# Optimization experiments

Hardware: AMD Instinct MI355X
Metric: run time of the kernel (lower is better)

## Reference

```python
import jax, jax.numpy as jnp
import numpy as np

R = 2          # pool ratio -> context window = R * P
P = 8          # patch_size
STRIDE = 8     # window_stride
NH = 8         # n_heads
EPS = 1e-6


def _partition_nonoverlap(x, ws):
    # (N,C,H,W) -> (N*nH*nW, C, ws, ws), matches F.unfold path with padding 0
    n, c, h, w = x.shape
    x = x.reshape(n, c, h // ws, ws, w // ws, ws)
    x = jnp.transpose(x, (0, 2, 4, 1, 3, 5))
    return x.reshape(-1, c, ws, ws)


def _partition_overlap(x, ws, stride):
    # (N,C,H,W) -> (N*nH*nW, C, ws, ws) with padding (ws-stride)//2, matching F.unfold
    n, c, h, w = x.shape
    pad = (ws - stride) // 2
    xp = jnp.pad(x, ((0, 0), (0, 0), (pad, pad), (pad, pad)))
    ih = (jnp.arange(h // stride) * stride)[:, None] + jnp.arange(ws)[None, :]
    iw = (jnp.arange(w // stride) * stride)[:, None] + jnp.arange(ws)[None, :]
    xw = xp[:, :, ih, :]          # (n, c, nH, ws, Wp)
    xw = xw[:, :, :, :, iw]       # (n, c, nH, ws, nW, ws)
    xw = jnp.transpose(xw, (0, 2, 4, 1, 3, 5))  # (n, nH, nW, c, ws, ws)
    return xw.reshape(-1, c, ws, ws)


def setup_inputs() -> dict:
    key = jax.random.key(0)
    ks = jax.random.split(key, 4)
    C = 512
    x = jax.random.normal(ks[0], (1, C, 128, 128), jnp.float32)
    ln_w = jnp.ones((C,), jnp.float32)
    ln_b = jnp.zeros((C,), jnp.float32)
    mix_w = jax.random.normal(ks[1], (NH, P * P, P * P), jnp.float32) * 0.02
    mix_b = jnp.zeros((NH, P * P), jnp.float32)
    in_w = jax.random.normal(ks[2], (3 * C, C), jnp.float32) * 0.02
    in_b = jnp.zeros((3 * C,), jnp.float32)
    out_w = jax.random.normal(ks[3], (C, C), jnp.float32) * 0.02
    out_b = jnp.zeros((C,), jnp.float32)
    return dict(x=x, ln_w=ln_w, ln_b=ln_b, mix_w=mix_w, mix_b=mix_b,
                in_w=in_w, in_b=in_b, out_w=out_w, out_b=out_b)


def reference(x, ln_w, ln_b, mix_w, mix_b, in_w, in_b, out_w, out_b):
    n, c, h, w = x.shape
    ws = R * P
    L = P * P  # 64 positions per window

    # query windows: non-overlapping 8x8 patches -> (B, L, C)
    q = _partition_nonoverlap(x, P)
    q = q.reshape(-1, c, L).transpose(0, 2, 1)

    # context windows: 16x16 overlapping, avg-pooled r x r -> 8x8 -> (B, L, C)
    ctx = _partition_overlap(x, ws, STRIDE)
    ctx = ctx.reshape(-1, c, P, R, P, R).mean(axis=(3, 5))  # AvgPool2d(r, r)
    ctx = ctx.reshape(-1, c, L).transpose(0, 2, 1)

    # LayerNorm over channel dim (eps 1e-6, biased variance)
    mu = ctx.mean(-1, keepdims=True)
    var = ctx.var(-1, keepdims=True)
    ctx = (ctx - mu) / jnp.sqrt(var + EPS) * ln_w + ln_b

    # PositionMixing: per-head Linear(64,64) over the L axis + residual
    B = ctx.shape[0]
    t = ctx.transpose(0, 2, 1).reshape(B, NH, c // NH, L)  # (B, H, hd, L)
    mixed = jnp.einsum('bhcl,hml->bhcm', t, mix_w) + mix_b[None, :, None, :]
    ctx = (t + mixed).reshape(B, c, L).transpose(0, 2, 1)  # (B, L, C)

    # nn.MultiheadAttention with batch_first=False (torch default):
    # first dim B (windows) is the SEQUENCE, second dim L=64 is the BATCH.
    hd = c // NH
    Wq, Wk, Wv = in_w[:c], in_w[c:2 * c], in_w[2 * c:]
    bq, bk, bv = in_b[:c], in_b[c:2 * c], in_b[2 * c:]
    Q = (jnp.einsum('slc,ec->sle', q, Wq) + bq).reshape(B, L, NH, hd)
    K = (jnp.einsum('slc,ec->sle', ctx, Wk) + bk).reshape(B, L, NH, hd)
    V = (jnp.einsum('slc,ec->sle', ctx, Wv) + bv).reshape(B, L, NH, hd)
    scale = 1.0 / jnp.sqrt(jnp.asarray(hd, x.dtype))
    scores = jnp.einsum('slhd,tlhd->lhst', Q, K) * scale  # (L, H, B, B)
    attn = jax.nn.softmax(scores, axis=-1)
    o = jnp.einsum('lhst,tlhd->slhd', attn, V).reshape(B, L, c)
    o = jnp.einsum('slc,ec->sle', o, out_w) + out_b

    # nlc_to_nchw + window_reverse -> (N, C, H, W)
    o = o.transpose(0, 2, 1).reshape(B, c, P, P)
    o = o.reshape(n, h // P, w // P, c, P, P)
    o = jnp.transpose(o, (0, 3, 1, 4, 2, 5)).reshape(n, c, h, w)
    return o
```

## Files before the change

### kernel.cpp

```cpp
#include <hip/hip_runtime.h>


typedef __bf16 bf16;
typedef __bf16 bf16x2 __attribute__((ext_vector_type(2)));
typedef __bf16 bf16x4 __attribute__((ext_vector_type(4)));
typedef __bf16 bf16x8 __attribute__((ext_vector_type(8)));
typedef float f32x4 __attribute__((ext_vector_type(4)));

#define MFMA(a, b, c) __builtin_amdgcn_mfma_f32_16x16x32_bf16(a, b, c, 0, 0, 0)

__device__ __forceinline__ void gll16(const void* g, void* l) {
  __builtin_amdgcn_global_load_lds((const __attribute__((address_space(1))) void*)g,
                                   (__attribute__((address_space(3))) void*)l, 16, 0, 0);
}

__global__ void k_wconv(const float* __restrict__ in_w, const float* __restrict__ out_w,
                        bf16* __restrict__ wib, bf16* __restrict__ wob) {
  int i = blockIdx.x * blockDim.x + threadIdx.x;
  const int n1 = (1536 * 512) / 4;
  float4 v;
  bf16* dst;
  if (i < n1) { v = ((const float4*)in_w)[i];      dst = wib + (size_t)i * 4; }
  else        { v = ((const float4*)out_w)[i - n1]; dst = wob + (size_t)(i - n1) * 4; }
  dst[0] = (bf16)v.x; dst[1] = (bf16)v.y; dst[2] = (bf16)v.z; dst[3] = (bf16)v.w;
}

__global__ __launch_bounds__(256) void k_pq(const float* __restrict__ x,
                                            float* __restrict__ xp2t,
                                            bf16* __restrict__ qb) {
  __shared__ float xs[2][64][133];
  const int y2 = blockIdx.x, c0 = blockIdx.y * 64, t = threadIdx.x;
  #pragma unroll
  for (int it = 0; it < 16; ++it) {
    int flat = it * 256 + t;
    int ci = flat >> 6, rest = flat & 63;
    int yb = rest >> 5, xq = rest & 31;
    float4 v = *(const float4*)(x + (size_t)(c0 + ci) * 16384 +
                                (size_t)(2 * y2 + yb) * 128 + xq * 4);
    float* d = &xs[yb][ci][xq * 4];
    d[0] = v.x; d[1] = v.y; d[2] = v.z; d[3] = v.w;
  }
  __syncthreads();
  #pragma unroll
  for (int it = 0; it < 16; ++it) {
    int flat = it * 256 + t;
    int x2 = flat >> 6, ci = flat & 63;
    float s = xs[0][ci][2 * x2] + xs[0][ci][2 * x2 + 1] +
              xs[1][ci][2 * x2] + xs[1][ci][2 * x2 + 1];
    xp2t[(size_t)(y2 * 64 + x2) * 512 + c0 + ci] = 0.25f * s;
  }
  #pragma unroll
  for (int yb = 0; yb < 2; ++yb) {
    const int Y = 2 * y2 + yb;
    const int hy = Y >> 3, py = Y & 7;
    #pragma unroll
    for (int it = 0; it < 32; ++it) {
      int flat = it * 256 + t;
      int X = flat >> 6, ci = flat & 63;
      int l = py * 8 + (X & 7), s = hy * 16 + (X >> 3);
      qb[((size_t)l * 256 + s) * 512 + c0 + ci] = (bf16)xs[yb][ci][X];
    }
  }
}

__global__ __launch_bounds__(512) void k_ln(const float* __restrict__ xp2t,
                                            const float* __restrict__ lnw,
                                            const float* __restrict__ lnb,
                                            bf16* __restrict__ T) {
  __shared__ bf16 Tt[512][24];
  const int s = blockIdx.x, qt = blockIdx.y;
  const int wy = s >> 4, wx = s & 15;
  const int t = threadIdx.x, wv = t >> 6, ln = t & 63;

  float wl[8], bl[8];
  #pragma unroll
  for (int k = 0; k < 8; ++k) { wl[k] = lnw[k * 64 + ln]; bl[k] = lnb[k * 64 + ln]; }

  float v[2][8], mu_[2], rs_[2];
  #pragma unroll
  for (int p = 0; p < 2; ++p) {
    const int l = qt * 16 + wv * 2 + p;
    const int py = l >> 3, px = l & 7;
    const int y2 = wy * 4 - 2 + py, x2 = wx * 4 - 2 + px;
    const bool inb = (y2 >= 0) && (y2 < 64) && (x2 >= 0) && (x2 < 64);
    const float* src = xp2t + (size_t)(y2 * 64 + x2) * 512;
    float sum = 0.f, ssq = 0.f;
    #pragma unroll
    for (int k = 0; k < 8; ++k) {
      float xv = 0.f;
      if (inb) xv = src[k * 64 + ln];
      v[p][k] = xv; sum += xv; ssq += xv * xv;
    }
    #pragma unroll
    for (int off = 1; off < 64; off <<= 1) {
      sum += __shfl_xor(sum, off);
      ssq += __shfl_xor(ssq, off);
    }
    float mu = sum * (1.f / 512.f);
    mu_[p] = mu;
    rs_[p] = rsqrtf(ssq * (1.f / 512.f) - mu * mu + 1e-6f);
  }
  #pragma unroll
  for (int k = 0; k < 8; ++k) {
    const int c = k * 64 + ln;
    bf16x2 u;
    u.x = (bf16)((v[0][k] - mu_[0]) * rs_[0] * wl[k] + bl[k]);
    u.y = (bf16)((v[1][k] - mu_[1]) * rs_[1] * wl[k] + bl[k]);
    *(bf16x2*)(&Tt[c][wv * 2]) = u;
  }
  __syncthreads();
  #pragma unroll
  for (int it = 0; it < 2; ++it) {
    int flat = it * 512 + t;
    int c = flat >> 1, ch = flat & 1;
    bf16x8 u = *(const bf16x8*)(&Tt[c][ch * 8]);
    *(bf16x8*)(T + ((size_t)s * 512 + c) * 64 + qt * 16 + ch * 8) = u;
  }
}

__global__ __launch_bounds__(256) void k_mix(const bf16* __restrict__ T,
                                             const float* __restrict__ mix_w,
                                             const float* __restrict__ mix_b,
                                             bf16* __restrict__ ctx) {
  const int t = threadIdx.x, wv = t >> 6, ln = t & 63;
  const int s = blockIdx.x, hg = blockIdx.y;
  const int h = hg * 4 + wv;
  const int q = ln >> 4, r = ln & 15;

  bf16x8 a[4][2];
  #pragma unroll
  for (int m = 0; m < 4; ++m) {
    #pragma unroll
    for (int ks = 0; ks < 2; ++ks) {
      const int rm = m * 16 + r;
      const float* wsrc = mix_w + ((size_t)h * 64 + rm) * 64 + ks * 32 + q * 8;
      bf16x8 pk;
      #pragma unroll
      for (int e = 0; e < 8; ++e) {
        int l = ks * 32 + q * 8 + e;
        float w = wsrc[e] + (rm == l ? 1.f : 0.f);
        pk[e] = (bf16)w;
      }
      a[m][ks] = pk;
    }
  }
  const bf16* Tb = T + ((size_t)s * 512 + h * 64) * 64;
  bf16x8 b[4][2];
  #pragma unroll
  for (int n = 0; n < 4; ++n) {
    #pragma unroll
    for (int ks = 0; ks < 2; ++ks)
      b[n][ks] = *(const bf16x8*)(Tb + (size_t)(n * 16 + r) * 64 + ks * 32 + q * 8);
  }
  f32x4 acc[4][4] = {};
  #pragma unroll
  for (int ks = 0; ks < 2; ++ks) {
    #pragma unroll
    for (int m = 0; m < 4; ++m) {
      #pragma unroll
      for (int n = 0; n < 4; ++n) acc[m][n] = MFMA(a[m][ks], b[n][ks], acc[m][n]);
    }
  }
  #pragma unroll
  for (int m = 0; m < 4; ++m) {
    #pragma unroll
    for (int j = 0; j < 4; ++j) {
      const int rm = m * 16 + q * 4 + j;
      const float bias = mix_b[h * 64 + rm];
      #pragma unroll
      for (int n = 0; n < 4; ++n)
        ctx[((size_t)rm * 256 + s) * 512 + h * 64 + n * 16 + r] =
            (bf16)(acc[m][n][j] + bias);
    }
  }
}

template <int MODE>
__global__ __launch_bounds__(256, 4) void k_gemm(const bf16* __restrict__ A,
                                                 const bf16* __restrict__ B,
                                                 const float* __restrict__ bias,
                                                 bf16* __restrict__ O0,
                                                 bf16* __restrict__ O1) {
  __shared__ bf16 As[8192];
  __shared__ bf16 Bs[8192];
  const int t = threadIdx.x, wv = t >> 6, ln = t & 63;
  const int bm = blockIdx.x, bn = blockIdx.y;
  const int wm = wv >> 1, wn = wv & 1;
  const int q = ln >> 4, r = ln & 15;
  f32x4 acc[4][4] = {};

  const int srow = wv * 8 + (ln >> 3);
  const int swzc = (ln & 7) ^ (ln >> 3);
  const char* ga = (const char*)A + ((size_t)(bm * 128 + srow) * 512) * 2 + swzc * 16;
  const char* gb = (const char*)B + ((size_t)(bn * 128 + srow) * 512) * 2 + swzc * 16;

  for (int k0 = 0; k0 < 512; k0 += 64) {
    #pragma unroll
    for (int i = 0; i < 4; ++i) {
      gll16(ga + (size_t)i * 32 * 1024 + k0 * 2, As + i * 2048 + wv * 512);
      gll16(gb + (size_t)i * 32 * 1024 + k0 * 2, Bs + i * 2048 + wv * 512);
    }
    __syncthreads();
    #pragma unroll
    for (int ks = 0; ks < 2; ++ks) {
      bf16x8 af[4], bfr[4];
      #pragma unroll
      for (int m = 0; m < 4; ++m)
        af[m] = *(const bf16x8*)(As + (wm * 64 + m * 16 + r) * 64 +
                                 (((ks * 4 + q) ^ (r & 7)) * 8));
      #pragma unroll
      for (int n = 0; n < 4; ++n)
        bfr[n] = *(const bf16x8*)(Bs + (wn * 64 + n * 16 + r) * 64 +
                                  (((ks * 4 + q) ^ (r & 7)) * 8));
      #pragma unroll
      for (int m = 0; m < 4; ++m) {
        #pragma unroll
        for (int n = 0; n < 4; ++n) acc[m][n] = MFMA(af[m], bfr[n], acc[m][n]);
      }
    }
    __syncthreads();
  }

  const int r0 = bm * 128 + wm * 64 + q * 4;
  const int c0 = bn * 128 + wn * 64 + r;
  #pragma unroll
  for (int m = 0; m < 4; ++m) {
    const int rg0 = r0 + m * 16;
    #pragma unroll
    for (int n = 0; n < 4; ++n) {
      const int cg = c0 + n * 16;
      const float bv = bias[cg];
      if constexpr (MODE == 2) {
        #pragma unroll
        for (int j = 0; j < 4; ++j)
          O0[(size_t)(rg0 + j) * 512 + cg] = (bf16)(acc[m][n][j] + bv);
      } else if constexpr (MODE == 0) {
        const int li = rg0 >> 8;
        #pragma unroll
        for (int j = 0; j < 4; ++j) {
          int sp = (rg0 + j) & 255;
          O0[(((size_t)li * 8 + (cg >> 6)) * 256 + sp) * 64 + (cg & 63)] =
              (bf16)(acc[m][n][j] + bv);
        }
      } else {
        const int li = rg0 >> 8;
        if (cg < 512) {
          #pragma unroll
          for (int j = 0; j < 4; ++j) {
            int sp = (rg0 + j) & 255;
            O0[(((size_t)li * 8 + (cg >> 6)) * 256 + sp) * 64 + (cg & 63)] =
                (bf16)(acc[m][n][j] + bv);
          }
        } else {
          const int e = cg - 512, hh = e >> 6, d = e & 63;
          const int sp = rg0 & 255;
          bf16x4 pk;
          #pragma unroll
          for (int j = 0; j < 4; ++j) pk[j] = (bf16)(acc[m][n][j] + bv);
          *(bf16x4*)(&O1[(((size_t)li * 8 + hh) * 64 + d) * 256 + sp]) = pk;
        }
      }
    }
  }
}

__global__ __launch_bounds__(256, 4) void k_attn(const bf16* __restrict__ Qa,
                                                 const bf16* __restrict__ Ka,
                                                 const bf16* __restrict__ Vt,
                                                 bf16* __restrict__ Oa) {
  __shared__ bf16 Ks[128][68];
  __shared__ bf16 Ps[64][132];
  __shared__ float sfl[64];
  __shared__ float rrs[64];

  const int t = threadIdx.x, wv = t >> 6, ln = t & 63;
  const int q = ln >> 4, r = ln & 15;
  const int bid = blockIdx.x;
  const int st = (bid >> 3) & 3;
  const int lh = (bid & 7) | ((bid >> 5) << 3);
  const int s0 = st * 64;
  const size_t base = (size_t)lh * (256 * 64);
  const bf16* Qlh = Qa + base;
  const bf16* Klh = Ka + base;
  const bf16* Vlh = Vt + base;

  const float SC = 0.125f * 1.4426950408889634f;

  bf16x8 aq[2];
  #pragma unroll
  for (int ks = 0; ks < 2; ++ks)
    aq[ks] = *(const bf16x8*)(Qlh + (size_t)(s0 + wv * 16 + r) * 64 + ks * 32 + q * 8);

  const int krow = t >> 1, khf = (t & 1) * 32;
  {
    bf16x8 kst0[4];
    #pragma unroll
    for (int i = 0; i < 4; ++i)
      kst0[i] = *(const bf16x8*)(Klh + (size_t)krow * 64 + khf + i * 8);
    #pragma unroll
    for (int i = 0; i < 4; ++i) *(bf16x8*)(&Ks[krow][khf + i * 8]) = kst0[i];
  }
  __syncthreads();

  f32x4 ao[4] = {};
  float m4[4], l4[4];
  f32x4 acc[8];

  #pragma unroll
  for (int n = 0; n < 8; ++n) acc[n] = (f32x4){0.f, 0.f, 0.f, 0.f};
  __builtin_amdgcn_s_setprio(1);
  #pragma unroll
  for (int n = 0; n < 8; ++n) {
    bf16x8 b0 = *(const bf16x8*)(&Ks[n * 16 + r][q * 8]);
    bf16x8 b1 = *(const bf16x8*)(&Ks[n * 16 + r][32 + q * 8]);
    acc[n] = MFMA(aq[0], b0, acc[n]);
    acc[n] = MFMA(aq[1], b1, acc[n]);
  }
  __builtin_amdgcn_s_setprio(0);

  bf16x8 bv[4];
  #pragma unroll
  for (int ks = 0; ks < 4; ++ks)
    bv[ks] = *(const bf16x8*)(Vlh + (size_t)(wv * 16 + r) * 256 + ks * 32 + q * 8);
  bf16x8 kst[4];
  #pragma unroll
  for (int i = 0; i < 4; ++i)
    kst[i] = *(const bf16x8*)(Klh + (size_t)(128 + krow) * 64 + khf + i * 8);

  #pragma unroll
  for (int j = 0; j < 4; ++j) {
    float mx = acc[0][j];
    #pragma unroll
    for (int n = 1; n < 8; ++n) mx = fmaxf(mx, acc[n][j]);
    #pragma unroll
    for (int off = 1; off < 16; off <<= 1) mx = fmaxf(mx, __shfl_xor(mx, off));
    m4[j] = mx;
    const float ms = mx * SC;
    float sm = 0.f;
    #pragma unroll
    for (int n = 0; n < 8; ++n) {
      float p = exp2f(acc[n][j] * SC - ms);
      acc[n][j] = p;
      sm += p;
    }
    #pragma unroll
    for (int off = 1; off < 16; off <<= 1) sm += __shfl_xor(sm, off);
    l4[j] = sm;
    const int row = wv * 16 + q * 4 + j;
    #pragma unroll
    for (int n = 0; n < 8; ++n) Ps[row][n * 16 + r] = (bf16)acc[n][j];
  }
  __syncthreads();

  #pragma unroll
  for (int i = 0; i < 4; ++i) *(bf16x8*)(&Ks[krow][khf + i * 8]) = kst[i];
  __builtin_amdgcn_s_setprio(1);
  #pragma unroll
  for (int ks = 0; ks < 4; ++ks) {
    #pragma unroll
    for (int m = 0; m < 4; ++m) {
      bf16x8 ap = *(const bf16x8*)(&Ps[m * 16 + r][ks * 32 + q * 8]);
      ao[m] = MFMA(ap, bv[ks], ao[m]);
    }
  }
  __builtin_amdgcn_s_setprio(0);
  __syncthreads();

  #pragma unroll
  for (int n = 0; n < 8; ++n) acc[n] = (f32x4){0.f, 0.f, 0.f, 0.f};
  __builtin_amdgcn_s_setprio(1);
  #pragma unroll
  for (int n = 0; n < 8; ++n) {
    bf16x8 b0 = *(const bf16x8*)(&Ks[n * 16 + r][q * 8]);
    bf16x8 b1 = *(const bf16x8*)(&Ks[n * 16 + r][32 + q * 8]);
    acc[n] = MFMA(aq[0], b0, acc[n]);
    acc[n] = MFMA(aq[1], b1, acc[n]);
  }
  __builtin_amdgcn_s_setprio(0);
  #pragma unroll
  for (int ks = 0; ks < 4; ++ks)
    bv[ks] = *(const bf16x8*)(Vlh + (size_t)(wv * 16 + r) * 256 + 128 + ks * 32 + q * 8);

  float sf4[4], rr4[4];
  #pragma unroll
  for (int j = 0; j < 4; ++j) {
    float mx = acc[0][j];
    #pragma unroll
    for (int n = 1; n < 8; ++n) mx = fmaxf(mx, acc[n][j]);
    #pragma unroll
    for (int off = 1; off < 16; off <<= 1) mx = fmaxf(mx, __shfl_xor(mx, off));
    const float mn = fmaxf(m4[j], mx);
    const float sf = exp2f((m4[j] - mn) * SC);
    const float ms = mn * SC;
    float sm = 0.f;
    #pragma unroll
    for (int n = 0; n < 8; ++n) {
      float p = exp2f(acc[n][j] * SC - ms);
      acc[n][j] = p;
      sm += p;
    }
    #pragma unroll
    for (int off = 1; off < 16; off <<= 1) sm += __shfl_xor(sm, off);
    sf4[j] = sf;
    rr4[j] = 1.f / (l4[j] * sf + sm);
    const int row = wv * 16 + q * 4 + j;
    #pragma unroll
    for (int n = 0; n < 8; ++n) Ps[row][n * 16 + r] = (bf16)acc[n][j];
  }
  if (r == 0) {
    *(f32x4*)(&sfl[wv * 16 + q * 4]) = (f32x4){sf4[0], sf4[1], sf4[2], sf4[3]};
    *(f32x4*)(&rrs[wv * 16 + q * 4]) = (f32x4){rr4[0], rr4[1], rr4[2], rr4[3]};
  }
  __syncthreads();

  #pragma unroll
  for (int m = 0; m < 4; ++m) {
    f32x4 sv = *(const f32x4*)(&sfl[m * 16 + q * 4]);
    #pragma unroll
    for (int j = 0; j < 4; ++j) ao[m][j] *= sv[j];
  }
  __builtin_amdgcn_s_setprio(1);
  #pragma unroll
  for (int ks = 0; ks < 4; ++ks) {
    #pragma unroll
    for (int m = 0; m < 4; ++m) {
      bf16x8 ap = *(const bf16x8*)(&Ps[m * 16 + r][ks * 32 + q * 8]);
      ao[m] = MFMA(ap, bv[ks], ao[m]);
    }
  }
  __builtin_amdgcn_s_setprio(0);

  float(*FS)[68] = (float(*)[68])(&Ks[0][0]);
  #pragma unroll
  for (int m = 0; m < 4; ++m) {
    f32x4 rv = *(const f32x4*)(&rrs[m * 16 + q * 4]);
    #pragma unroll
    for (int j = 0; j < 4; ++j)
      FS[m * 16 + q * 4 + j][wv * 16 + r] = ao[m][j] * rv[j];
  }
  __syncthreads();

  {
    const int row = t >> 2, qq = t & 3;
    const float* srcp = &FS[row][qq * 16];
    bf16x8 o0, o1;
    #pragma unroll
    for (int i = 0; i < 8; ++i) o0[i] = (bf16)srcp[i];
    #pragma unroll
    for (int i = 0; i < 8; ++i) o1[i] = (bf16)srcp[8 + i];
    bf16* dst = Oa + ((size_t)(lh >> 3) * 256 + s0 + row) * 512 + (lh & 7) * 64 + qq * 16;
    *(bf16x8*)(dst) = o0;
    *(bf16x8*)(dst + 8) = o1;
  }
}

__global__ void k_orelay(const bf16* __restrict__ o_tmp, float* __restrict__ out) {
  __shared__ bf16 buf[64][130];
  const int hy = blockIdx.x, py = blockIdx.y, e0 = blockIdx.z * 64, t = threadIdx.x;
  #pragma unroll
  for (int i = 0; i < 32; ++i) {
    int flat = i * 256 + t;
    int r = flat >> 6, e = flat & 63;
    int px = r >> 4, hx = r & 15;
    buf[e][hx * 8 + px] =
        o_tmp[((size_t)(py * 8 + px) * 256 + hy * 16 + hx) * 512 + e0 + e];
  }
  __syncthreads();
  const int Y = hy * 8 + py;
  #pragma unroll
  for (int i = 0; i < 32; ++i) {
    int flat = i * 256 + t;
    int e = flat >> 7, X = flat & 127;
    out[(size_t)(e0 + e) * 16384 + (size_t)Y * 128 + X] = (float)buf[e][X];
  }
}

extern "C" void kernel_launch(void* const* d_in, const int* in_sizes, int n_in,
                              void* d_out, int out_size, void* d_ws, size_t ws_size,
                              hipStream_t stream) {
  const float* x     = (const float*)d_in[0];
  const float* ln_w  = (const float*)d_in[1];
  const float* ln_b  = (const float*)d_in[2];
  const float* mix_w = (const float*)d_in[3];
  const float* mix_b = (const float*)d_in[4];
  const float* in_w  = (const float*)d_in[5];
  const float* in_b  = (const float*)d_in[6];
  const float* out_w = (const float*)d_in[7];
  const float* out_b = (const float*)d_in[8];
  float* out = (float*)d_out;
  char* ws = (char*)d_ws;

  const size_t MB = 1u << 20;
  float* xp2t = (float*)(ws);
  bf16* qb    = (bf16*)(ws + 8 * MB);
  bf16* Tn    = (bf16*)(ws + 24 * MB);
  bf16* ctxb  = (bf16*)(ws + 40 * MB);
  bf16* Qa    = (bf16*)(ws + 56 * MB);
  bf16* Ka    = (bf16*)(ws);
  bf16* Vt    = (bf16*)(ws + 16 * MB);
  bf16* oatt  = (bf16*)(ws + 32 * MB);
  bf16* otmp  = (bf16*)(ws + 48 * MB);
  bf16* wib   = (bf16*)(ws + 72 * MB);
  bf16* wob   = (bf16*)(ws + 72 * MB + 1572864);

  k_wconv<<<1024, 256, 0, stream>>>(in_w, out_w, wib, wob);
  k_pq<<<dim3(64, 8), 256, 0, stream>>>(x, xp2t, qb);
  k_ln<<<dim3(256, 4), 512, 0, stream>>>(xp2t, ln_w, ln_b, Tn);
  k_mix<<<dim3(256, 2), 256, 0, stream>>>(Tn, mix_w, mix_b, ctxb);
  k_gemm<0><<<dim3(128, 4), 256, 0, stream>>>(qb, wib, in_b, Qa, nullptr);
  k_gemm<1><<<dim3(128, 8), 256, 0, stream>>>(ctxb, wib + 512 * 512, in_b + 512, Ka, Vt);
  k_attn<<<2048, 256, 0, stream>>>(Qa, Ka, Vt, oatt);
  k_gemm<2><<<dim3(128, 4), 256, 0, stream>>>(oatt, wob, out_b, otmp, nullptr);
  k_orelay<<<dim3(16, 8, 8), 256, 0, stream>>>(otmp, out);
}
```

Measured before the change: 138.1 us.

## Merge Q and KV projection GEMMs into one launch; restructure attention into 4-chunk double-buffered loop

The Q projection and the K/V projection GEMMs are merged into a single launch with a 12-wide grid, where blocks choose their inputs by blockIdx.y. This removes one launch and lets the two GEMMs share the GPU. The attention kernel now processes keys in four 64-key chunks with a double-buffered K tile in shared memory and an online softmax. This shrinks LDS and register use so occupancy can rise to 5 blocks per CU, at the cost of more barriers and more rescaling steps per block.

```diff
diff --git a/kernel.cpp b/kernel.cpp
--- a/kernel.cpp
+++ b/kernel.cpp
@@ -175,12 +175,98 @@
   }
 }
 
-template <int MODE>
-__global__ __launch_bounds__(256, 4) void k_gemm(const bf16* __restrict__ A,
-                                                 const bf16* __restrict__ B,
-                                                 const float* __restrict__ bias,
-                                                 bf16* __restrict__ O0,
-                                                 bf16* __restrict__ O1) {
+__global__ __launch_bounds__(256, 4) void k_gemmQKV(const bf16* __restrict__ qb,
+                                                    const bf16* __restrict__ ctxb,
+                                                    const bf16* __restrict__ wib,
+                                                    const float* __restrict__ in_b,
+                                                    bf16* __restrict__ Qa,
+                                                    bf16* __restrict__ Ka,
+                                                    bf16* __restrict__ Vt) {
+  __shared__ bf16 As[8192];
+  __shared__ bf16 Bs[8192];
+  const int t = threadIdx.x, wv = t >> 6, ln = t & 63;
+  const int bm = blockIdx.x, bny = blockIdx.y;
+  const bool isQ = (bny < 4);
+  const int bn = isQ ? bny : bny - 4;
+  const bf16* A = isQ ? qb : ctxb;
+  const bf16* B = isQ ? wib : wib + 512 * 512;
+  const float* bias = isQ ? in_b : in_b + 512;
+  const int wm = wv >> 1, wn = wv & 1;
+  const int q = ln >> 4, r = ln & 15;
+  f32x4 acc[4][4] = {};
+
+  const int srow = wv * 8 + (ln >> 3);
+  const int swzc = (ln & 7) ^ (ln >> 3);
+  const char* ga = (const char*)A + ((size_t)(bm * 128 + srow) * 512) * 2 + swzc * 16;
+  const char* gb = (const char*)B + ((size_t)(bn * 128 + srow) * 512) * 2 + swzc * 16;
+
+  for (int k0 = 0; k0 < 512; k0 += 64) {
+    #pragma unroll
+    for (int i = 0; i < 4; ++i) {
+      gll16(ga + (size_t)i * 32 * 1024 + k0 * 2, As + i * 2048 + wv * 512);
+      gll16(gb + (size_t)i * 32 * 1024 + k0 * 2, Bs + i * 2048 + wv * 512);
+    }
+    __syncthreads();
+    #pragma unroll
+    for (int ks = 0; ks < 2; ++ks) {
+      bf16x8 af[4], bfr[4];
+      #pragma unroll
+      for (int m = 0; m < 4; ++m)
+        af[m] = *(const bf16x8*)(As + (wm * 64 + m * 16 + r) * 64 +
+                                 (((ks * 4 + q) ^ (r & 7)) * 8));
+      #pragma unroll
+      for (int n = 0; n < 4; ++n)
+        bfr[n] = *(const bf16x8*)(Bs + (wn * 64 + n * 16 + r) * 64 +
+                                  (((ks * 4 + q) ^ (r & 7)) * 8));
+      #pragma unroll
+      for (int m = 0; m < 4; ++m) {
+        #pragma unroll
+        for (int n = 0; n < 4; ++n) acc[m][n] = MFMA(af[m], bfr[n], acc[m][n]);
+      }
+    }
+    __syncthreads();
+  }
+
+  const int r0 = bm * 128 + wm * 64 + q * 4;
+  const int c0 = bn * 128 + wn * 64 + r;
+  #pragma unroll
+  for (int m = 0; m < 4; ++m) {
+    const int rg0 = r0 + m * 16;
+    const int li = rg0 >> 8;
+    #pragma unroll
+    for (int n = 0; n < 4; ++n) {
+      const int cg = c0 + n * 16;
+      const float bv = bias[cg];
+      if (isQ) {
+        #pragma unroll
+        for (int j = 0; j < 4; ++j) {
+          int sp = (rg0 + j) & 255;
+          Qa[(((size_t)li * 8 + (cg >> 6)) * 256 + sp) * 64 + (cg & 63)] =
+              (bf16)(acc[m][n][j] + bv);
+        }
+      } else if (cg < 512) {
+        #pragma unroll
+        for (int j = 0; j < 4; ++j) {
+          int sp = (rg0 + j) & 255;
+          Ka[(((size_t)li * 8 + (cg >> 6)) * 256 + sp) * 64 + (cg & 63)] =
+              (bf16)(acc[m][n][j] + bv);
+        }
+      } else {
+        const int e = cg - 512, hh = e >> 6, d = e & 63;
+        const int sp = rg0 & 255;
+        bf16x4 pk;
+        #pragma unroll
+        for (int j = 0; j < 4; ++j) pk[j] = (bf16)(acc[m][n][j] + bv);
+        *(bf16x4*)(&Vt[(((size_t)li * 8 + hh) * 64 + d) * 256 + sp]) = pk;
+      }
+    }
+  }
+}
+
+__global__ __launch_bounds__(256, 4) void k_gemmO(const bf16* __restrict__ A,
+                                                  const bf16* __restrict__ B,
+                                                  const float* __restrict__ bias,
+                                                  bf16* __restrict__ O0) {
   __shared__ bf16 As[8192];
   __shared__ bf16 Bs[8192];
   const int t = threadIdx.x, wv = t >> 6, ln = t & 63;
@@ -230,46 +316,19 @@
     for (int n = 0; n < 4; ++n) {
       const int cg = c0 + n * 16;
       const float bv = bias[cg];
-      if constexpr (MODE == 2) {
-        #pragma unroll
-        for (int j = 0; j < 4; ++j)
-          O0[(size_t)(rg0 + j) * 512 + cg] = (bf16)(acc[m][n][j] + bv);
-      } else if constexpr (MODE == 0) {
-        const int li = rg0 >> 8;
-        #pragma unroll
-        for (int j = 0; j < 4; ++j) {
-          int sp = (rg0 + j) & 255;
-          O0[(((size_t)li * 8 + (cg >> 6)) * 256 + sp) * 64 + (cg & 63)] =
-              (bf16)(acc[m][n][j] + bv);
-        }
-      } else {
-        const int li = rg0 >> 8;
-        if (cg < 512) {
-          #pragma unroll
-          for (int j = 0; j < 4; ++j) {
-            int sp = (rg0 + j) & 255;
-            O0[(((size_t)li * 8 + (cg >> 6)) * 256 + sp) * 64 + (cg & 63)] =
-                (bf16)(acc[m][n][j] + bv);
-          }
-        } else {
-          const int e = cg - 512, hh = e >> 6, d = e & 63;
-          const int sp = rg0 & 255;
-          bf16x4 pk;
-          #pragma unroll
-          for (int j = 0; j < 4; ++j) pk[j] = (bf16)(acc[m][n][j] + bv);
-          *(bf16x4*)(&O1[(((size_t)li * 8 + hh) * 64 + d) * 256 + sp]) = pk;
-        }
-      }
-    }
-  }
-}
-
-__global__ __launch_bounds__(256, 4) void k_attn(const bf16* __restrict__ Qa,
+      #pragma unroll
+      for (int j = 0; j < 4; ++j)
+        O0[(size_t)(rg0 + j) * 512 + cg] = (bf16)(acc[m][n][j] + bv);
+    }
+  }
+}
+
+__global__ __launch_bounds__(256, 5) void k_attn(const bf16* __restrict__ Qa,
                                                  const bf16* __restrict__ Ka,
                                                  const bf16* __restrict__ Vt,
                                                  bf16* __restrict__ Oa) {
-  __shared__ bf16 Ks[128][68];
-  __shared__ bf16 Ps[64][132];
+  __shared__ bf16 Ks[2][64][68];
+  __shared__ bf16 Ps[64][68];
   __shared__ float sfl[64];
   __shared__ float rrs[64];
 
@@ -283,7 +342,6 @@
   const bf16* Qlh = Qa + base;
   const bf16* Klh = Ka + base;
   const bf16* Vlh = Vt + base;
-
   const float SC = 0.125f * 1.4426950408889634f;
 
   bf16x8 aq[2];
@@ -291,146 +349,110 @@
   for (int ks = 0; ks < 2; ++ks)
     aq[ks] = *(const bf16x8*)(Qlh + (size_t)(s0 + wv * 16 + r) * 64 + ks * 32 + q * 8);
 
-  const int krow = t >> 1, khf = (t & 1) * 32;
+  const int krow = t >> 2, kc = (t & 3) * 16;
   {
-    bf16x8 kst0[4];
-    #pragma unroll
-    for (int i = 0; i < 4; ++i)
-      kst0[i] = *(const bf16x8*)(Klh + (size_t)krow * 64 + khf + i * 8);
-    #pragma unroll
-    for (int i = 0; i < 4; ++i) *(bf16x8*)(&Ks[krow][khf + i * 8]) = kst0[i];
+    const bf16* k0p = Klh + (size_t)krow * 64 + kc;
+    bf16x8 a0 = *(const bf16x8*)(k0p);
+    bf16x8 a1 = *(const bf16x8*)(k0p + 8);
+    *(bf16x8*)(&Ks[0][krow][kc]) = a0;
+    *(bf16x8*)(&Ks[0][krow][kc + 8]) = a1;
   }
   __syncthreads();
 
   f32x4 ao[4] = {};
   float m4[4], l4[4];
-  f32x4 acc[8];
-
-  #pragma unroll
-  for (int n = 0; n < 8; ++n) acc[n] = (f32x4){0.f, 0.f, 0.f, 0.f};
-  __builtin_amdgcn_s_setprio(1);
-  #pragma unroll
-  for (int n = 0; n < 8; ++n) {
-    bf16x8 b0 = *(const bf16x8*)(&Ks[n * 16 + r][q * 8]);
-    bf16x8 b1 = *(const bf16x8*)(&Ks[n * 16 + r][32 + q * 8]);
-    acc[n] = MFMA(aq[0], b0, acc[n]);
-    acc[n] = MFMA(aq[1], b1, acc[n]);
-  }
-  __builtin_amdgcn_s_setprio(0);
-
-  bf16x8 bv[4];
-  #pragma unroll
-  for (int ks = 0; ks < 4; ++ks)
-    bv[ks] = *(const bf16x8*)(Vlh + (size_t)(wv * 16 + r) * 256 + ks * 32 + q * 8);
-  bf16x8 kst[4];
-  #pragma unroll
-  for (int i = 0; i < 4; ++i)
-    kst[i] = *(const bf16x8*)(Klh + (size_t)(128 + krow) * 64 + khf + i * 8);
-
-  #pragma unroll
-  for (int j = 0; j < 4; ++j) {
-    float mx = acc[0][j];
-    #pragma unroll
-    for (int n = 1; n < 8; ++n) mx = fmaxf(mx, acc[n][j]);
-    #pragma unroll
-    for (int off = 1; off < 16; off <<= 1) mx = fmaxf(mx, __shfl_xor(mx, off));
-    m4[j] = mx;
-    const float ms = mx * SC;
-    float sm = 0.f;
-    #pragma unroll
-    for (int n = 0; n < 8; ++n) {
-      float p = exp2f(acc[n][j] * SC - ms);
-      acc[n][j] = p;
-      sm += p;
-    }
-    #pragma unroll
-    for (int off = 1; off < 16; off <<= 1) sm += __shfl_xor(sm, off);
-    l4[j] = sm;
-    const int row = wv * 16 + q * 4 + j;
-    #pragma unroll
-    for (int n = 0; n < 8; ++n) Ps[row][n * 16 + r] = (bf16)acc[n][j];
-  }
-  __syncthreads();
-
-  #pragma unroll
-  for (int i = 0; i < 4; ++i) *(bf16x8*)(&Ks[krow][khf + i * 8]) = kst[i];
-  __builtin_amdgcn_s_setprio(1);
-  #pragma unroll
-  for (int ks = 0; ks < 4; ++ks) {
-    #pragma unroll
-    for (int m = 0; m < 4; ++m) {
-      bf16x8 ap = *(const bf16x8*)(&Ps[m * 16 + r][ks * 32 + q * 8]);
-      ao[m] = MFMA(ap, bv[ks], ao[m]);
-    }
-  }
-  __builtin_amdgcn_s_setprio(0);
-  __syncthreads();
-
-  #pragma unroll
-  for (int n = 0; n < 8; ++n) acc[n] = (f32x4){0.f, 0.f, 0.f, 0.f};
-  __builtin_amdgcn_s_setprio(1);
-  #pragma unroll
-  for (int n = 0; n < 8; ++n) {
-    bf16x8 b0 = *(const bf16x8*)(&Ks[n * 16 + r][q * 8]);
-    bf16x8 b1 = *(const bf16x8*)(&Ks[n * 16 + r][32 + q * 8]);
-    acc[n] = MFMA(aq[0], b0, acc[n]);
-    acc[n] = MFMA(aq[1], b1, acc[n]);
-  }
-  __builtin_amdgcn_s_setprio(0);
-  #pragma unroll
-  for (int ks = 0; ks < 4; ++ks)
-    bv[ks] = *(const bf16x8*)(Vlh + (size_t)(wv * 16 + r) * 256 + 128 + ks * 32 + q * 8);
-
-  float sf4[4], rr4[4];
-  #pragma unroll
-  for (int j = 0; j < 4; ++j) {
-    float mx = acc[0][j];
-    #pragma unroll
-    for (int n = 1; n < 8; ++n) mx = fmaxf(mx, acc[n][j]);
-    #pragma unroll
-    for (int off = 1; off < 16; off <<= 1) mx = fmaxf(mx, __shfl_xor(mx, off));
-    const float mn = fmaxf(m4[j], mx);
-    const float sf = exp2f((m4[j] - mn) * SC);
-    const float ms = mn * SC;
-    float sm = 0.f;
-    #pragma unroll
-    for (int n = 0; n < 8; ++n) {
-      float p = exp2f(acc[n][j] * SC - ms);
-      acc[n][j] = p;
-      sm += p;
-    }
-    #pragma unroll
-    for (int off = 1; off < 16; off <<= 1) sm += __shfl_xor(sm, off);
-    sf4[j] = sf;
-    rr4[j] = 1.f / (l4[j] * sf + sm);
-    const int row = wv * 16 + q * 4 + j;
-    #pragma unroll
-    for (int n = 0; n < 8; ++n) Ps[row][n * 16 + r] = (bf16)acc[n][j];
-  }
-  if (r == 0) {
-    *(f32x4*)(&sfl[wv * 16 + q * 4]) = (f32x4){sf4[0], sf4[1], sf4[2], sf4[3]};
-    *(f32x4*)(&rrs[wv * 16 + q * 4]) = (f32x4){rr4[0], rr4[1], rr4[2], rr4[3]};
-  }
-  __syncthreads();
-
-  #pragma unroll
-  for (int m = 0; m < 4; ++m) {
-    f32x4 sv = *(const f32x4*)(&sfl[m * 16 + q * 4]);
-    #pragma unroll
-    for (int j = 0; j < 4; ++j) ao[m][j] *= sv[j];
-  }
-  __builtin_amdgcn_s_setprio(1);
-  #pragma unroll
-  for (int ks = 0; ks < 4; ++ks) {
-    #pragma unroll
-    for (int m = 0; m < 4; ++m) {
-      bf16x8 ap = *(const bf16x8*)(&Ps[m * 16 + r][ks * 32 + q * 8]);
-      ao[m] = MFMA(ap, bv[ks], ao[m]);
-    }
-  }
-  __builtin_amdgcn_s_setprio(0);
-
-  float(*FS)[68] = (float(*)[68])(&Ks[0][0]);
+
+  #pragma unroll
+  for (int it = 0; it < 4; ++it) {
+    const int cur = it & 1;
+
+    f32x4 acc[4] = {};
+    __builtin_amdgcn_s_setprio(1);
+    #pragma unroll
+    for (int n = 0; n < 4; ++n) {
+      bf16x8 b0 = *(const bf16x8*)(&Ks[cur][n * 16 + r][q * 8]);
+      bf16x8 b1 = *(const bf16x8*)(&Ks[cur][n * 16 + r][32 + q * 8]);
+      acc[n] = MFMA(aq[0], b0, acc[n]);
+      acc[n] = MFMA(aq[1], b1, acc[n]);
+    }
+    __builtin_amdgcn_s_setprio(0);
+
+    bf16x8 kp0, kp1;
+    if (it < 3) {
+      const bf16* kn = Klh + (size_t)(it + 1) * 4096 + (size_t)krow * 64 + kc;
+      kp0 = *(const bf16x8*)(kn);
+      kp1 = *(const bf16x8*)(kn + 8);
+    }
+    const bf16* vp = Vlh + (size_t)(wv * 16 + r) * 256 + it * 64 + q * 8;
+    bf16x8 bv0 = *(const bf16x8*)(vp);
+    bf16x8 bv1 = *(const bf16x8*)(vp + 32);
+
+    float sf4[4];
+    #pragma unroll
+    for (int j = 0; j < 4; ++j) {
+      float mx = fmaxf(fmaxf(acc[0][j], acc[1][j]), fmaxf(acc[2][j], acc[3][j]));
+      #pragma unroll
+      for (int off = 1; off < 16; off <<= 1) mx = fmaxf(mx, __shfl_xor(mx, off));
+      const float mnew = (it == 0) ? mx : fmaxf(m4[j], mx);
+      const float ms = mnew * SC;
+      float sm = 0.f;
+      #pragma unroll
+      for (int n = 0; n < 4; ++n) {
+        float p = exp2f(acc[n][j] * SC - ms);
+        acc[n][j] = p;
+        sm += p;
+      }
+      #pragma unroll
+      for (int off = 1; off < 16; off <<= 1) sm += __shfl_xor(sm, off);
+      if (it == 0) {
+        m4[j] = mnew; l4[j] = sm; sf4[j] = 1.f;
+      } else {
+        const float sf = exp2f(m4[j] * SC - ms);
+        l4[j] = l4[j] * sf + sm;
+        m4[j] = mnew;
+        sf4[j] = sf;
+      }
+      const int row = wv * 16 + q * 4 + j;
+      #pragma unroll
+      for (int n = 0; n < 4; ++n) Ps[row][n * 16 + r] = (bf16)acc[n][j];
+    }
+    if (it > 0 && r == 0)
+      *(f32x4*)(&sfl[wv * 16 + q * 4]) = (f32x4){sf4[0], sf4[1], sf4[2], sf4[3]};
+    if (it == 3 && r == 0) {
+      f32x4 rv;
+      #pragma unroll
+      for (int j = 0; j < 4; ++j) rv[j] = 1.f / l4[j];
+      *(f32x4*)(&rrs[wv * 16 + q * 4]) = rv;
+    }
+    if (it < 3) {
+      *(bf16x8*)(&Ks[cur ^ 1][krow][kc]) = kp0;
+      *(bf16x8*)(&Ks[cur ^ 1][krow][kc + 8]) = kp1;
+    }
+    __syncthreads();
+
+    if (it > 0) {
+      #pragma unroll
+      for (int m = 0; m < 4; ++m) {
+        f32x4 sv = *(const f32x4*)(&sfl[m * 16 + q * 4]);
+        #pragma unroll
+        for (int j = 0; j < 4; ++j) ao[m][j] *= sv[j];
+      }
+    }
+    __builtin_amdgcn_s_setprio(1);
+    #pragma unroll
+    for (int ks = 0; ks < 2; ++ks) {
+      bf16x8 bvv = ks ? bv1 : bv0;
+      #pragma unroll
+      for (int m = 0; m < 4; ++m) {
+        bf16x8 ap = *(const bf16x8*)(&Ps[m * 16 + r][ks * 32 + q * 8]);
+        ao[m] = MFMA(ap, bvv, ao[m]);
+      }
+    }
+    __builtin_amdgcn_s_setprio(0);
+    if (it < 3) __syncthreads();
+  }
+
+  float(*FS)[68] = (float(*)[68])(&Ks[0][0][0]);
   #pragma unroll
   for (int m = 0; m < 4; ++m) {
     f32x4 rv = *(const f32x4*)(&rrs[m * 16 + q * 4]);
@@ -439,7 +461,6 @@
       FS[m * 16 + q * 4 + j][wv * 16 + r] = ao[m][j] * rv[j];
   }
   __syncthreads();
-
   {
     const int row = t >> 2, qq = t & 3;
     const float* srcp = &FS[row][qq * 16];
@@ -507,9 +528,8 @@
   k_pq<<<dim3(64, 8), 256, 0, stream>>>(x, xp2t, qb);
   k_ln<<<dim3(256, 4), 512, 0, stream>>>(xp2t, ln_w, ln_b, Tn);
   k_mix<<<dim3(256, 2), 256, 0, stream>>>(Tn, mix_w, mix_b, ctxb);
-  k_gemm<0><<<dim3(128, 4), 256, 0, stream>>>(qb, wib, in_b, Qa, nullptr);
-  k_gemm<1><<<dim3(128, 8), 256, 0, stream>>>(ctxb, wib + 512 * 512, in_b + 512, Ka, Vt);
+  k_gemmQKV<<<dim3(128, 12), 256, 0, stream>>>(qb, ctxb, wib, in_b, Qa, Ka, Vt);
   k_attn<<<2048, 256, 0, stream>>>(Qa, Ka, Vt, oatt);
-  k_gemm<2><<<dim3(128, 4), 256, 0, stream>>>(oatt, wob, out_b, otmp, nullptr);
+  k_gemmO<<<dim3(128, 4), 256, 0, stream>>>(oatt, wob, out_b, otmp);
   k_orelay<<<dim3(16, 8, 8), 256, 0, stream>>>(otmp, out);
 }
```

Measured after the change: 148.2 us. +7.3%, slower.
